# Performance work log

Hardware: AMD Instinct MI355X
Metric: run time of the kernel (lower is better)

The kernel has to match this reference:

```python
import jax, jax.numpy as jnp
import numpy as np

NUM_HEADS = 16

def setup_inputs() -> dict:
    key = jax.random.key(0)
    ks = jax.random.split(key, 5)
    B, T, C = 2, 2048, 1024
    s = 0.02
    return {
        "x": jax.random.normal(ks[0], (B, T, C), dtype=jnp.float32),
        "in_w": jax.random.normal(ks[1], (3 * C, C), dtype=jnp.float32) * s,
        "in_b": jax.random.normal(ks[2], (3 * C,), dtype=jnp.float32) * s,
        "out_w": jax.random.normal(ks[3], (C, C), dtype=jnp.float32) * s,
        "out_b": jax.random.normal(ks[4], (C,), dtype=jnp.float32) * s,
    }

def reference(x, in_w, in_b, out_w, out_b):
    B, T, C = x.shape
    H = NUM_HEADS
    D = C // H
    qvk = x @ in_w.T + in_b  # (B, T, 3C)
    # einops 'b t (d k h) -> k b h t d': factor 3C as (D, 3, H), D outermost
    qvk = qvk.reshape(B, T, D, 3, H).transpose(3, 0, 4, 1, 2)  # (3, B, H, T, D)
    q, v, k = qvk[0], qvk[1], qvk[2]  # note q, v, k assignment order
    scores = jnp.einsum('bhid,bhjd->bhij', q, k) * (D ** -0.5)  # (B, H, T, T)
    causal = jnp.tril(jnp.ones((T, T), dtype=bool))
    scores = jnp.where(causal, scores, -jnp.inf)
    attn = jax.nn.softmax(scores, axis=-1)
    out = jnp.einsum('bhij,bhjd->bhid', attn, v)  # (B, H, T, D)
    out = out.transpose(0, 2, 1, 3).reshape(B, T, C)  # 'b h t d -> b t (h d)'
    return out @ out_w.T + out_b
```

## Files before the change

kernel.cpp:

```cpp
#include <hip/hip_runtime.h>


#define BB 2
#define TT 2048
#define CC 1024
#define HH 16
#define DD 64
#define MM (BB*TT)
#define N3 (3*CC)
#define BH (BB*HH)

typedef unsigned short u16;
typedef unsigned int   u32;
typedef __bf16 bf16x8 __attribute__((ext_vector_type(8)));
typedef float  f32x4  __attribute__((ext_vector_type(4)));

__device__ __forceinline__ float bf16_lo(u32 u) { return __uint_as_float(u << 16); }
__device__ __forceinline__ float bf16_hi(u32 u) { return __uint_as_float(u & 0xffff0000u); }
__device__ __forceinline__ u16 f32_to_bf16(float f) {
  u32 u = __float_as_uint(f);
  u32 r = (u + 0x7fffu + ((u >> 16) & 1u)) >> 16;
  return (u16)r;
}

__global__ __launch_bounds__(256) void cast_f32_bf16(const float* __restrict__ src,
                                                     u16* __restrict__ dst, int n4) {
  int i = blockIdx.x * 256 + threadIdx.x;
  if (i < n4) {
    float4 f = reinterpret_cast<const float4*>(src)[i];
    uint2 pk;
    pk.x = (u32)f32_to_bf16(f.x) | ((u32)f32_to_bf16(f.y) << 16);
    pk.y = (u32)f32_to_bf16(f.z) | ((u32)f32_to_bf16(f.w) << 16);
    reinterpret_cast<uint2*>(dst)[i] = pk;
  }
}

__device__ __forceinline__ void gemm_core(const u16* __restrict__ Ag,
                                          const u16* __restrict__ Bg,
                                          int K, u16* Al, u16* Bl,
                                          int m0, int n0, f32x4 acc[4][4]) {
  const int tid = threadIdx.x, lane = tid & 63, w = tid >> 6;
  const int quad = lane >> 4, colr = lane & 15;
  const int mw = (w >> 1) * 64, nw = (w & 1) * 64;
  const int srow = lane >> 3, scol = lane & 7;
  const uint4* Al4 = reinterpret_cast<const uint4*>(Al);
  const uint4* Bl4 = reinterpret_cast<const uint4*>(Bl);
  for (int kt = 0; kt < K / 64; ++kt) {
    __syncthreads();
    #pragma unroll
    for (int ii = 0; ii < 4; ++ii) {
      int inst = w * 4 + ii;
      int row = inst * 8 + srow;
      int cs = scol ^ (row & 7);
      const u16* ga = Ag + (size_t)(m0 + row) * K + kt * 64 + cs * 8;
      const u16* gb = Bg + (size_t)(n0 + row) * K + kt * 64 + cs * 8;
      __builtin_amdgcn_global_load_lds(
          (const __attribute__((address_space(1))) void*)ga,
          (__attribute__((address_space(3))) void*)(Al + inst * 512), 16, 0, 0);
      __builtin_amdgcn_global_load_lds(
          (const __attribute__((address_space(1))) void*)gb,
          (__attribute__((address_space(3))) void*)(Bl + inst * 512), 16, 0, 0);
    }
    __syncthreads();
    #pragma unroll
    for (int ks = 0; ks < 2; ++ks) {
      bf16x8 af[4], bfr[4];
      #pragma unroll
      for (int t = 0; t < 4; ++t) {
        int mrow = mw + t * 16 + colr;
        af[t]  = __builtin_bit_cast(bf16x8, Al4[mrow * 8 + ((ks * 4 + quad) ^ (mrow & 7))]);
        int nrow = nw + t * 16 + colr;
        bfr[t] = __builtin_bit_cast(bf16x8, Bl4[nrow * 8 + ((ks * 4 + quad) ^ (nrow & 7))]);
      }
      #pragma unroll
      for (int mt = 0; mt < 4; ++mt)
        #pragma unroll
        for (int nt = 0; nt < 4; ++nt)
          acc[mt][nt] = __builtin_amdgcn_mfma_f32_16x16x32_bf16(af[mt], bfr[nt], acc[mt][nt], 0, 0, 0);
    }
  }
}

__global__ __launch_bounds__(256) void gemm_qkv(const u16* __restrict__ xb,
                                                const u16* __restrict__ wb,
                                                const float* __restrict__ in_b,
                                                u16* __restrict__ Y) {
  __shared__ __align__(16) u16 Al[128 * 64];
  __shared__ __align__(16) u16 Bl[128 * 64];
  const int lane = threadIdx.x & 63, w = threadIdx.x >> 6;
  const int quad = lane >> 4, colr = lane & 15;
  const int mw = (w >> 1) * 64, nw = (w & 1) * 64;
  const int m0 = blockIdx.x * 128, n0 = blockIdx.y * 128;
  f32x4 acc[4][4];
  #pragma unroll
  for (int mt = 0; mt < 4; ++mt)
    #pragma unroll
    for (int nt = 0; nt < 4; ++nt) acc[mt][nt] = (f32x4){0.f, 0.f, 0.f, 0.f};
  gemm_core(xb, wb, CC, Al, Bl, m0, n0, acc);
  float bias[4];
  #pragma unroll
  for (int nt = 0; nt < 4; ++nt) bias[nt] = in_b[n0 + nw + nt * 16 + colr];
  #pragma unroll
  for (int mt = 0; mt < 4; ++mt)
    #pragma unroll
    for (int e = 0; e < 4; ++e) {
      int row = m0 + mw + mt * 16 + quad * 4 + e;
      #pragma unroll
      for (int nt = 0; nt < 4; ++nt)
        Y[(size_t)row * N3 + n0 + nw + nt * 16 + colr] = f32_to_bf16(acc[mt][nt][e] + bias[nt]);
    }
}

__global__ __launch_bounds__(256) void repack_qkv(const u16* __restrict__ Y,
                                                  u16* __restrict__ qkv) {
  __shared__ __align__(16) u16 Yl[N3];
  const int m = blockIdx.x, tid = threadIdx.x;
  const int b_ = m >> 11, t = m & (TT - 1);
  const uint4* Yg = reinterpret_cast<const uint4*>(Y + (size_t)m * N3);
  uint4* Yl4 = reinterpret_cast<uint4*>(Yl);
  for (int i = tid; i < N3 / 8; i += 256) Yl4[i] = Yg[i];
  __syncthreads();
  for (int it = tid; it < 768; it += 256) {
    int h = it & 15, s = (it >> 4) % 3, dg = it / 48;
    int col = s * 16 + h;
    u32 lo = (u32)Yl[(dg * 4 + 0) * 48 + col] | ((u32)Yl[(dg * 4 + 1) * 48 + col] << 16);
    u32 hi = (u32)Yl[(dg * 4 + 2) * 48 + col] | ((u32)Yl[(dg * 4 + 3) * 48 + col] << 16);
    uint2 pk; pk.x = lo; pk.y = hi;
    size_t base = (((size_t)s * BH + b_ * HH + h) * TT + t) * DD + dg * 4;
    *reinterpret_cast<uint2*>(qkv + base) = pk;
  }
}

__global__ __launch_bounds__(256, 2) void attn_mfma(const u16* __restrict__ qkv,
                                                    u16* __restrict__ aout) {
  __shared__ __align__(16) u32   Kl[64 * 36];
  __shared__ __align__(16) u32   Vt[64 * 36];
  __shared__ __align__(16) float Pl[4 * 16 * 68];
  const int tid  = threadIdx.x;
  const int lane = tid & 63, w = tid >> 6;
  const int quad = lane >> 4, colr = lane & 15;
  const int bh = blockIdx.y;
  const int b_ = bh >> 4, h = bh & 15;

  const uint4* Qg4 = reinterpret_cast<const uint4*>(qkv + (size_t)bh * TT * DD);
  const uint4* Vg4 = reinterpret_cast<const uint4*>(qkv + ((size_t)BH + bh) * TT * DD);
  const uint4* Kg4 = reinterpret_cast<const uint4*>(qkv + ((size_t)2 * BH + bh) * TT * DD);
  uint4* Kl4 = reinterpret_cast<uint4*>(Kl);
  const uint4* Vt4 = reinterpret_cast<const uint4*>(Vt);
  const float4* Pl4 = reinterpret_cast<const float4*>(Pl);

  const int s_jp = tid & 31, s_oct = tid >> 5;
  const int wbase = w * (16 * 68);

  for (int pass = 0; pass < 2; ++pass) {
    const int qt = pass ? (31 - (int)blockIdx.x) : (int)blockIdx.x;
    const int i0 = qt * 64;

    bf16x8 qa[2];
    {
      size_t qrow = (size_t)(i0 + w * 16 + colr) * 8;
      qa[0] = __builtin_bit_cast(bf16x8, Qg4[qrow + quad]);
      qa[1] = __builtin_bit_cast(bf16x8, Qg4[qrow + 4 + quad]);
    }
    f32x4 oacc[4];
    #pragma unroll
    for (int dt = 0; dt < 4; ++dt) oacc[dt] = (f32x4){0.f, 0.f, 0.f, 0.f};
    float lpart = 0.f;

    for (int jt = 0; jt <= qt; ++jt) {
      const int j0 = jt * 64;
      __syncthreads();
      #pragma unroll
      for (int it = 0; it < 2; ++it) {
        int idx = it * 256 + tid;
        int jj = idx >> 3, oc = idx & 7;
        Kl4[jj * 9 + oc] = Kg4[(size_t)(j0 + jj) * 8 + oc];
      }
      {
        int j = j0 + s_jp * 2;
        uint4 va = Vg4[(size_t)j * 8 + s_oct];
        uint4 vb = Vg4[(size_t)(j + 1) * 8 + s_oct];
        u32 aw[4] = {va.x, va.y, va.z, va.w};
        u32 bw[4] = {vb.x, vb.y, vb.z, vb.w};
        #pragma unroll
        for (int e = 0; e < 8; ++e) {
          u32 lo = (e & 1) ? (aw[e >> 1] >> 16)         : (aw[e >> 1] & 0xffffu);
          u32 hi = (e & 1) ? (bw[e >> 1] & 0xffff0000u) : (bw[e >> 1] << 16);
          Vt[(s_oct * 8 + e) * 36 + s_jp] = lo | hi;
        }
      }
      __syncthreads();

      f32x4 sacc[4];
      #pragma unroll
      for (int t4 = 0; t4 < 4; ++t4) sacc[t4] = (f32x4){0.f, 0.f, 0.f, 0.f};
      #pragma unroll
      for (int t4 = 0; t4 < 4; ++t4) {
        #pragma unroll
        for (int ks = 0; ks < 2; ++ks) {
          bf16x8 kb = __builtin_bit_cast(bf16x8,
              reinterpret_cast<const uint4*>(Kl)[(t4 * 16 + colr) * 9 + ks * 4 + quad]);
          sacc[t4] = __builtin_amdgcn_mfma_f32_16x16x32_bf16(qa[ks], kb, sacc[t4], 0, 0, 0);
        }
      }

      const bool diag = (jt == qt);
      #pragma unroll
      for (int t4 = 0; t4 < 4; ++t4) {
        #pragma unroll
        for (int rg = 0; rg < 4; ++rg) {
          float p = __expf(sacc[t4][rg] * 0.125f);
          if (diag && (t4 * 16 + colr > w * 16 + quad * 4 + rg)) p = 0.f;
          Pl[wbase + (quad * 4 + rg) * 68 + t4 * 16 + colr] = p;
        }
      }

      bf16x8 pa[2];
      #pragma unroll
      for (int ks = 0; ks < 2; ++ks) {
        int b4 = (wbase + colr * 68 + ks * 32 + quad * 8) >> 2;
        float4 f0 = Pl4[b4], f1 = Pl4[b4 + 1];
        lpart += ((f0.x + f0.y) + (f0.z + f0.w)) + ((f1.x + f1.y) + (f1.z + f1.w));
        uint4 u;
        u.x = (u32)f32_to_bf16(f0.x) | ((u32)f32_to_bf16(f0.y) << 16);
        u.y = (u32)f32_to_bf16(f0.z) | ((u32)f32_to_bf16(f0.w) << 16);
        u.z = (u32)f32_to_bf16(f1.x) | ((u32)f32_to_bf16(f1.y) << 16);
        u.w = (u32)f32_to_bf16(f1.z) | ((u32)f32_to_bf16(f1.w) << 16);
        pa[ks] = __builtin_bit_cast(bf16x8, u);
      }

      #pragma unroll
      for (int dt = 0; dt < 4; ++dt) {
        #pragma unroll
        for (int ks = 0; ks < 2; ++ks) {
          bf16x8 vb = __builtin_bit_cast(bf16x8, Vt4[(dt * 16 + colr) * 9 + ks * 4 + quad]);
          oacc[dt] = __builtin_amdgcn_mfma_f32_16x16x32_bf16(pa[ks], vb, oacc[dt], 0, 0, 0);
        }
      }
    }

    float lsum = lpart;
    lsum += __shfl_xor(lsum, 16);
    lsum += __shfl_xor(lsum, 32);
    float linv[4];
    #pragma unroll
    for (int rg = 0; rg < 4; ++rg)
      linv[rg] = 1.0f / __shfl(lsum, quad * 4 + rg);
    #pragma unroll
    for (int dt = 0; dt < 4; ++dt) {
      #pragma unroll
      for (int rg = 0; rg < 4; ++rg) {
        int ig = i0 + w * 16 + quad * 4 + rg;
        size_t off = ((size_t)(b_ * TT + ig)) * CC + h * DD + dt * 16 + colr;
        aout[off] = f32_to_bf16(oacc[dt][rg] * linv[rg]);
      }
    }
  }
}

__global__ __launch_bounds__(256) void gemm_out(const u16* __restrict__ ab,
                                                const u16* __restrict__ owb,
                                                const float* __restrict__ out_b,
                                                float* __restrict__ out) {
  __shared__ __align__(16) u16 Al[128 * 64];
  __shared__ __align__(16) u16 Bl[128 * 64];
  const int lane = threadIdx.x & 63, w = threadIdx.x >> 6;
  const int quad = lane >> 4, colr = lane & 15;
  const int mw = (w >> 1) * 64, nw = (w & 1) * 64;
  const int m0 = blockIdx.x * 128, n0 = blockIdx.y * 128;
  f32x4 acc[4][4];
  #pragma unroll
  for (int mt = 0; mt < 4; ++mt)
    #pragma unroll
    for (int nt = 0; nt < 4; ++nt) acc[mt][nt] = (f32x4){0.f, 0.f, 0.f, 0.f};
  gemm_core(ab, owb, CC, Al, Bl, m0, n0, acc);
  float bias[4];
  #pragma unroll
  for (int nt = 0; nt < 4; ++nt) bias[nt] = out_b[n0 + nw + nt * 16 + colr];
  #pragma unroll
  for (int mt = 0; mt < 4; ++mt)
    #pragma unroll
    for (int e = 0; e < 4; ++e) {
      int row = m0 + mw + mt * 16 + quad * 4 + e;
      #pragma unroll
      for (int nt = 0; nt < 4; ++nt)
        out[(size_t)row * CC + n0 + nw + nt * 16 + colr] = acc[mt][nt][e] + bias[nt];
    }
}

extern "C" void kernel_launch(void* const* d_in, const int* in_sizes, int n_in,
                              void* d_out, int out_size, void* d_ws, size_t ws_size,
                              hipStream_t stream) {
  const float* x     = (const float*)d_in[0];
  const float* in_w  = (const float*)d_in[1];
  const float* in_b  = (const float*)d_in[2];
  const float* out_w = (const float*)d_in[3];
  const float* out_b = (const float*)d_in[4];
  float* out = (float*)d_out;

  char* ws = (char*)d_ws;
  u16* xb  = (u16*)(ws + 0);
  u16* ab  = (u16*)(ws + 0);
  u16* wb  = (u16*)(ws + 8388608);
  u16* owb = (u16*)(ws + 14680064);
  u16* Y   = (u16*)(ws + 16777216);
  u16* qkv = (u16*)(ws + 41943040);

  cast_f32_bf16<<<dim3(MM * CC / 4 / 256), 256, 0, stream>>>(x, xb, MM * CC / 4);
  cast_f32_bf16<<<dim3(N3 * CC / 4 / 256), 256, 0, stream>>>(in_w, wb, N3 * CC / 4);
  cast_f32_bf16<<<dim3(CC * CC / 4 / 256), 256, 0, stream>>>(out_w, owb, CC * CC / 4);

  gemm_qkv<<<dim3(MM / 128, N3 / 128), 256, 0, stream>>>(xb, wb, in_b, Y);
  repack_qkv<<<dim3(MM), 256, 0, stream>>>(Y, qkv);
  attn_mfma<<<dim3(16, BH), 256, 0, stream>>>(qkv, ab);
  gemm_out<<<dim3(MM / 128, CC / 128), 256, 0, stream>>>(ab, owb, out_b, out);
}
```

Baseline: 236.1 us.

## Enlarge attention query tile to 128 rows and load K straight to registers

The attention kernel now handles 128 query rows per block: each warp owns 32 rows, so every K and V fragment feeds two MFMAs. K fragments are read from global memory into registers instead of staging through LDS. The next V tile is prefetched while the current one is used. The grid becomes 256 flattened blocks with a remapped (batch-head, query-tile) order, and cheaper exp2, perm-based packing and round-half-up bf16 conversion are used. The cost is higher register and LDS use, the dropped occupancy hint in launch bounds, and slightly different rounding.

New measurement: 231.5 us. Within noise of the previous version (-1.9%).

```diff
diff --git a/kernel.cpp b/kernel.cpp
--- a/kernel.cpp
+++ b/kernel.cpp
@@ -15,12 +15,17 @@
 typedef __bf16 bf16x8 __attribute__((ext_vector_type(8)));
 typedef float  f32x4  __attribute__((ext_vector_type(4)));
 
-__device__ __forceinline__ float bf16_lo(u32 u) { return __uint_as_float(u << 16); }
-__device__ __forceinline__ float bf16_hi(u32 u) { return __uint_as_float(u & 0xffff0000u); }
 __device__ __forceinline__ u16 f32_to_bf16(float f) {
   u32 u = __float_as_uint(f);
-  u32 r = (u + 0x7fffu + ((u >> 16) & 1u)) >> 16;
-  return (u16)r;
+  return (u16)((u + 0x7fffu + ((u >> 16) & 1u)) >> 16);
+}
+__device__ __forceinline__ u16 f32_to_bf16_fast(float f) {
+  return (u16)((__float_as_uint(f) + 0x8000u) >> 16);
+}
+__device__ __forceinline__ u32 pack2_bf16(float a, float b) {
+  u32 ua = __float_as_uint(a) + 0x8000u;
+  u32 ub = __float_as_uint(b) + 0x8000u;
+  return __builtin_amdgcn_perm(ub, ua, 0x07060302);
 }
 
 __global__ __launch_bounds__(256) void cast_f32_bf16(const float* __restrict__ src,
@@ -131,129 +136,146 @@
   }
 }
 
-__global__ __launch_bounds__(256, 2) void attn_mfma(const u16* __restrict__ qkv,
-                                                    u16* __restrict__ aout) {
-  __shared__ __align__(16) u32   Kl[64 * 36];
+__global__ __launch_bounds__(256) void attn_mfma(const u16* __restrict__ qkv,
+                                                 u16* __restrict__ aout) {
   __shared__ __align__(16) u32   Vt[64 * 36];
-  __shared__ __align__(16) float Pl[4 * 16 * 68];
+  __shared__ __align__(16) float Pl[4 * 32 * 68];
   const int tid  = threadIdx.x;
   const int lane = tid & 63, w = tid >> 6;
   const int quad = lane >> 4, colr = lane & 15;
-  const int bh = blockIdx.y;
+  const int flat = blockIdx.x;
+  const int bh = (flat & 7) * 4 + (flat >> 6);
+  const int pr = (flat >> 3) & 7;
   const int b_ = bh >> 4, h = bh & 15;
 
   const uint4* Qg4 = reinterpret_cast<const uint4*>(qkv + (size_t)bh * TT * DD);
   const uint4* Vg4 = reinterpret_cast<const uint4*>(qkv + ((size_t)BH + bh) * TT * DD);
   const uint4* Kg4 = reinterpret_cast<const uint4*>(qkv + ((size_t)2 * BH + bh) * TT * DD);
-  uint4* Kl4 = reinterpret_cast<uint4*>(Kl);
-  const uint4* Vt4 = reinterpret_cast<const uint4*>(Vt);
+  const uint4*  Vt4 = reinterpret_cast<const uint4*>(Vt);
   const float4* Pl4 = reinterpret_cast<const float4*>(Pl);
 
   const int s_jp = tid & 31, s_oct = tid >> 5;
-  const int wbase = w * (16 * 68);
+  const int wbase = w * (32 * 68);
 
   for (int pass = 0; pass < 2; ++pass) {
-    const int qt = pass ? (31 - (int)blockIdx.x) : (int)blockIdx.x;
-    const int i0 = qt * 64;
-
-    bf16x8 qa[2];
-    {
-      size_t qrow = (size_t)(i0 + w * 16 + colr) * 8;
-      qa[0] = __builtin_bit_cast(bf16x8, Qg4[qrow + quad]);
-      qa[1] = __builtin_bit_cast(bf16x8, Qg4[qrow + 4 + quad]);
-    }
-    f32x4 oacc[4];
-    #pragma unroll
-    for (int dt = 0; dt < 4; ++dt) oacc[dt] = (f32x4){0.f, 0.f, 0.f, 0.f};
-    float lpart = 0.f;
-
-    for (int jt = 0; jt <= qt; ++jt) {
+    const int qt = pass ? (15 - pr) : pr;
+    const int i0 = qt * 128;
+    const int jmax = 2 * qt + 1;
+
+    bf16x8 qa[2][2];
+    #pragma unroll
+    for (int u = 0; u < 2; ++u)
+      #pragma unroll
+      for (int ks = 0; ks < 2; ++ks)
+        qa[u][ks] = __builtin_bit_cast(bf16x8,
+            Qg4[(size_t)(i0 + w * 32 + u * 16 + colr) * 8 + ks * 4 + quad]);
+
+    f32x4 oacc[2][4];
+    #pragma unroll
+    for (int u = 0; u < 2; ++u)
+      #pragma unroll
+      for (int dt = 0; dt < 4; ++dt) oacc[u][dt] = (f32x4){0.f, 0.f, 0.f, 0.f};
+    float lp[2] = {0.f, 0.f};
+
+    uint4 va = Vg4[(size_t)(2 * s_jp) * 8 + s_oct];
+    uint4 vb = Vg4[(size_t)(2 * s_jp + 1) * 8 + s_oct];
+
+    for (int jt = 0; jt <= jmax; ++jt) {
       const int j0 = jt * 64;
+      uint4 kraw[4][2];
+      #pragma unroll
+      for (int t4 = 0; t4 < 4; ++t4)
+        #pragma unroll
+        for (int ks = 0; ks < 2; ++ks)
+          kraw[t4][ks] = Kg4[(size_t)(j0 + t4 * 16 + colr) * 8 + ks * 4 + quad];
+
       __syncthreads();
-      #pragma unroll
-      for (int it = 0; it < 2; ++it) {
-        int idx = it * 256 + tid;
-        int jj = idx >> 3, oc = idx & 7;
-        Kl4[jj * 9 + oc] = Kg4[(size_t)(j0 + jj) * 8 + oc];
-      }
       {
-        int j = j0 + s_jp * 2;
-        uint4 va = Vg4[(size_t)j * 8 + s_oct];
-        uint4 vb = Vg4[(size_t)(j + 1) * 8 + s_oct];
         u32 aw[4] = {va.x, va.y, va.z, va.w};
         u32 bw[4] = {vb.x, vb.y, vb.z, vb.w};
         #pragma unroll
-        for (int e = 0; e < 8; ++e) {
-          u32 lo = (e & 1) ? (aw[e >> 1] >> 16)         : (aw[e >> 1] & 0xffffu);
-          u32 hi = (e & 1) ? (bw[e >> 1] & 0xffff0000u) : (bw[e >> 1] << 16);
-          Vt[(s_oct * 8 + e) * 36 + s_jp] = lo | hi;
+        for (int m = 0; m < 4; ++m) {
+          Vt[(s_oct * 8 + 2 * m)     * 36 + s_jp] = __builtin_amdgcn_perm(bw[m], aw[m], 0x05040100);
+          Vt[(s_oct * 8 + 2 * m + 1) * 36 + s_jp] = __builtin_amdgcn_perm(bw[m], aw[m], 0x07060302);
         }
       }
       __syncthreads();
-
-      f32x4 sacc[4];
-      #pragma unroll
-      for (int t4 = 0; t4 < 4; ++t4) sacc[t4] = (f32x4){0.f, 0.f, 0.f, 0.f};
-      #pragma unroll
-      for (int t4 = 0; t4 < 4; ++t4) {
+      if (jt < jmax) {
+        int nj = j0 + 64;
+        va = Vg4[(size_t)(nj + 2 * s_jp) * 8 + s_oct];
+        vb = Vg4[(size_t)(nj + 2 * s_jp + 1) * 8 + s_oct];
+      }
+
+      f32x4 sacc[2][4];
+      #pragma unroll
+      for (int u = 0; u < 2; ++u)
+        #pragma unroll
+        for (int t4 = 0; t4 < 4; ++t4) sacc[u][t4] = (f32x4){0.f, 0.f, 0.f, 0.f};
+      #pragma unroll
+      for (int t4 = 0; t4 < 4; ++t4)
         #pragma unroll
         for (int ks = 0; ks < 2; ++ks) {
-          bf16x8 kb = __builtin_bit_cast(bf16x8,
-              reinterpret_cast<const uint4*>(Kl)[(t4 * 16 + colr) * 9 + ks * 4 + quad]);
-          sacc[t4] = __builtin_amdgcn_mfma_f32_16x16x32_bf16(qa[ks], kb, sacc[t4], 0, 0, 0);
-        }
-      }
-
-      const bool diag = (jt == qt);
-      #pragma unroll
-      for (int t4 = 0; t4 < 4; ++t4) {
+          bf16x8 kb = __builtin_bit_cast(bf16x8, kraw[t4][ks]);
+          #pragma unroll
+          for (int u = 0; u < 2; ++u)
+            sacc[u][t4] = __builtin_amdgcn_mfma_f32_16x16x32_bf16(qa[u][ks], kb, sacc[u][t4], 0, 0, 0);
+        }
+
+      const bool maskt = (jt >= 2 * qt);
+      const int joff = (jt - 2 * qt) * 64;
+      #pragma unroll
+      for (int u = 0; u < 2; ++u)
+        #pragma unroll
+        for (int t4 = 0; t4 < 4; ++t4)
+          #pragma unroll
+          for (int rg = 0; rg < 4; ++rg) {
+            float p = __builtin_amdgcn_exp2f(sacc[u][t4][rg] * 0.18033688011112042f);
+            if (maskt && (joff + t4 * 16 + colr > w * 32 + u * 16 + quad * 4 + rg)) p = 0.f;
+            Pl[wbase + (u * 16 + quad * 4 + rg) * 68 + t4 * 16 + colr] = p;
+          }
+
+      bf16x8 pa[2][2];
+      #pragma unroll
+      for (int u = 0; u < 2; ++u)
+        #pragma unroll
+        for (int ks = 0; ks < 2; ++ks) {
+          int b4 = (wbase + (u * 16 + colr) * 68 + ks * 32 + quad * 8) >> 2;
+          float4 f0 = Pl4[b4], f1 = Pl4[b4 + 1];
+          lp[u] += ((f0.x + f0.y) + (f0.z + f0.w)) + ((f1.x + f1.y) + (f1.z + f1.w));
+          uint4 up;
+          up.x = pack2_bf16(f0.x, f0.y); up.y = pack2_bf16(f0.z, f0.w);
+          up.z = pack2_bf16(f1.x, f1.y); up.w = pack2_bf16(f1.z, f1.w);
+          pa[u][ks] = __builtin_bit_cast(bf16x8, up);
+        }
+
+      #pragma unroll
+      for (int dt = 0; dt < 4; ++dt)
+        #pragma unroll
+        for (int ks = 0; ks < 2; ++ks) {
+          bf16x8 vfr = __builtin_bit_cast(bf16x8, Vt4[(dt * 16 + colr) * 9 + ks * 4 + quad]);
+          #pragma unroll
+          for (int u = 0; u < 2; ++u)
+            oacc[u][dt] = __builtin_amdgcn_mfma_f32_16x16x32_bf16(pa[u][ks], vfr, oacc[u][dt], 0, 0, 0);
+        }
+    }
+
+    #pragma unroll
+    for (int u = 0; u < 2; ++u) {
+      float ls = lp[u];
+      ls += __shfl_xor(ls, 16);
+      ls += __shfl_xor(ls, 32);
+      float linv[4];
+      #pragma unroll
+      for (int rg = 0; rg < 4; ++rg)
+        linv[rg] = 1.0f / __shfl(ls, quad * 4 + rg);
+      #pragma unroll
+      for (int dt = 0; dt < 4; ++dt)
         #pragma unroll
         for (int rg = 0; rg < 4; ++rg) {
-          float p = __expf(sacc[t4][rg] * 0.125f);
-          if (diag && (t4 * 16 + colr > w * 16 + quad * 4 + rg)) p = 0.f;
-          Pl[wbase + (quad * 4 + rg) * 68 + t4 * 16 + colr] = p;
-        }
-      }
-
-      bf16x8 pa[2];
-      #pragma unroll
-      for (int ks = 0; ks < 2; ++ks) {
-        int b4 = (wbase + colr * 68 + ks * 32 + quad * 8) >> 2;
-        float4 f0 = Pl4[b4], f1 = Pl4[b4 + 1];
-        lpart += ((f0.x + f0.y) + (f0.z + f0.w)) + ((f1.x + f1.y) + (f1.z + f1.w));
-        uint4 u;
-        u.x = (u32)f32_to_bf16(f0.x) | ((u32)f32_to_bf16(f0.y) << 16);
-        u.y = (u32)f32_to_bf16(f0.z) | ((u32)f32_to_bf16(f0.w) << 16);
-        u.z = (u32)f32_to_bf16(f1.x) | ((u32)f32_to_bf16(f1.y) << 16);
-        u.w = (u32)f32_to_bf16(f1.z) | ((u32)f32_to_bf16(f1.w) << 16);
-        pa[ks] = __builtin_bit_cast(bf16x8, u);
-      }
-
-      #pragma unroll
-      for (int dt = 0; dt < 4; ++dt) {
-        #pragma unroll
-        for (int ks = 0; ks < 2; ++ks) {
-          bf16x8 vb = __builtin_bit_cast(bf16x8, Vt4[(dt * 16 + colr) * 9 + ks * 4 + quad]);
-          oacc[dt] = __builtin_amdgcn_mfma_f32_16x16x32_bf16(pa[ks], vb, oacc[dt], 0, 0, 0);
-        }
-      }
-    }
-
-    float lsum = lpart;
-    lsum += __shfl_xor(lsum, 16);
-    lsum += __shfl_xor(lsum, 32);
-    float linv[4];
-    #pragma unroll
-    for (int rg = 0; rg < 4; ++rg)
-      linv[rg] = 1.0f / __shfl(lsum, quad * 4 + rg);
-    #pragma unroll
-    for (int dt = 0; dt < 4; ++dt) {
-      #pragma unroll
-      for (int rg = 0; rg < 4; ++rg) {
-        int ig = i0 + w * 16 + quad * 4 + rg;
-        size_t off = ((size_t)(b_ * TT + ig)) * CC + h * DD + dt * 16 + colr;
-        aout[off] = f32_to_bf16(oacc[dt][rg] * linv[rg]);
-      }
+          int ig = i0 + w * 32 + u * 16 + quad * 4 + rg;
+          size_t off = ((size_t)(b_ * TT + ig)) * CC + h * DD + dt * 16 + colr;
+          aout[off] = f32_to_bf16_fast(oacc[u][dt][rg] * linv[rg]);
+        }
     }
   }
 }
@@ -312,6 +334,6 @@
 
   gemm_qkv<<<dim3(MM / 128, N3 / 128), 256, 0, stream>>>(xb, wb, in_b, Y);
   repack_qkv<<<dim3(MM), 256, 0, stream>>>(Y, qkv);
-  attn_mfma<<<dim3(16, BH), 256, 0, stream>>>(qkv, ab);
+  attn_mfma<<<dim3(256), 256, 0, stream>>>(qkv, ab);
   gemm_out<<<dim3(MM / 128, CC / 128), 256, 0, stream>>>(ab, owb, out_b, out);
 }
```
